# Optimization experiments

Hardware: AMD Instinct MI355X
Metric: run time of the kernel (lower is better)

## Reference

```python
import jax, jax.numpy as jnp
import numpy as np

N, E, F, H, G, U, A = 50000, 800000, 96, 96, 64, 32, 16


def _linear_params(key, fan_in, fan_out):
    # torch nn.Linear default init: U(-1/sqrt(fan_in), 1/sqrt(fan_in))
    s = 1.0 / np.sqrt(fan_in)
    kw, kb = jax.random.split(key)
    W = jax.random.uniform(kw, (fan_in, fan_out), jnp.float32, -s, s)
    b = jax.random.uniform(kb, (fan_out,), jnp.float32, -s, s)
    return W, b


def setup_inputs() -> dict:
    key = jax.random.key(0)
    ks = jax.random.split(key, 12)
    x = jax.random.normal(ks[0], (N, F), jnp.float32)
    edge_index = jax.random.randint(ks[1], (2, E), 0, N, dtype=jnp.int32)
    batch = jnp.sort(jax.random.randint(ks[2], (N,), 0, G, dtype=jnp.int32))
    u = jax.random.normal(ks[3], (G, U), jnp.float32)
    W1, b1 = _linear_params(ks[4], F, H)      # conv1
    W2, b2 = _linear_params(ks[5], H, H)      # conv2
    aW1, ab1 = _linear_params(ks[6], H + U, H)
    aW2, ab2 = _linear_params(ks[7], H, A)
    cW1, cb1 = _linear_params(ks[8], H + U, H)
    cW2, cb2 = _linear_params(ks[9], H, 1)
    return {"x": x, "edge_index": edge_index, "batch": batch, "u": u,
            "W1": W1, "b1": b1, "W2": W2, "b2": b2,
            "aW1": aW1, "ab1": ab1, "aW2": aW2, "ab2": ab2,
            "cW1": cW1, "cb1": cb1, "cW2": cW2, "cb2": cb2}


def reference(x, edge_index, batch, u, W1, b1, W2, b2,
              aW1, ab1, aW2, ab2, cW1, cb1, cW2, cb2):
    n = x.shape[0]
    src, dst = edge_index[0], edge_index[1]
    # GCN symmetric normalization with self-loops (PyG GCNConv defaults)
    deg = jnp.zeros((n,), x.dtype).at[dst].add(1.0) + 1.0  # +1 for self-loop
    dis = jax.lax.rsqrt(deg)                               # deg^{-1/2}
    edge_norm = (dis[src] * dis[dst])[:, None]             # [E,1]
    self_norm = (dis * dis)[:, None]                       # [N,1] = deg^{-1}

    def gcn(h, W, b):
        h = h @ W                                          # linear (bias after agg)
        agg = jax.ops.segment_sum(h[src] * edge_norm, dst, num_segments=n)
        return agg + h * self_norm + b

    h = jax.nn.relu(gcn(x, W1, b1))
    h = jax.nn.relu(gcn(h, W2, b2))

    # global mean pool over graphs
    cnt = jax.ops.segment_sum(jnp.ones((n,), h.dtype), batch, num_segments=G)
    pooled = jax.ops.segment_sum(h, batch, num_segments=G) / jnp.maximum(cnt, 1.0)[:, None]

    comb = jnp.concatenate([pooled, u], axis=1)            # [G, H+U]
    action_logits = jax.nn.relu(comb @ aW1 + ab1) @ aW2 + ab2   # [G, A]
    state_value = jax.nn.relu(comb @ cW1 + cb1) @ cW2 + cb2     # [G, 1]
    return action_logits, state_value
```

## Files before the change

### kernel.cpp

```cpp
#include <hip/hip_runtime.h>
#include <hip/hip_bf16.h>

#define FH 96
#define GU 32
#define GA 16
#define NG 64

typedef __attribute__((ext_vector_type(8))) short bf16x8;
typedef __attribute__((ext_vector_type(8))) unsigned short u16x8;
typedef __attribute__((ext_vector_type(4))) float f32x4;

static __device__ __forceinline__ unsigned short f2bf(float f) {
    unsigned int u = __float_as_uint(f);
    unsigned int r = (u + 0x7fffu + ((u >> 16) & 1u)) >> 16;
    return (unsigned short)r;
}
static __device__ __forceinline__ float bf2f(unsigned short h) {
    return __uint_as_float(((unsigned int)h) << 16);
}

__global__ void zero_k(float4* __restrict__ p, int n4) {
    int i = blockIdx.x * blockDim.x + threadIdx.x;
    if (i < n4) p[i] = make_float4(0.f, 0.f, 0.f, 0.f);
}

__global__ void count_deg_k(const int* __restrict__ dst, int* __restrict__ deg,
                            unsigned short* __restrict__ rank16, int E) {
    int e = blockIdx.x * blockDim.x + threadIdx.x;
    if (e < E) rank16[e] = (unsigned short)atomicAdd(&deg[dst[e]], 1);
}

__global__ __launch_bounds__(256) void partial_k(const int* __restrict__ deg,
                                                 int* __restrict__ blockSums, int n) {
    int base = blockIdx.x * 1024;
    int t = threadIdx.x;
    int s = 0;
#pragma unroll
    for (int j = 0; j < 4; j++) {
        int i = base + t * 4 + j;
        if (i < n) s += deg[i];
    }
    __shared__ int red[4];
    for (int off = 32; off > 0; off >>= 1) s += __shfl_down(s, off, 64);
    if ((t & 63) == 0) red[t >> 6] = s;
    __syncthreads();
    if (t == 0) blockSums[blockIdx.x] = red[0] + red[1] + red[2] + red[3];
}

__global__ __launch_bounds__(256) void emit_k(const int* __restrict__ deg,
                                              const int* __restrict__ blockSums,
                                              int* __restrict__ rowstart,
                                              float* __restrict__ dis,
                                              int n, int nb) {
    __shared__ int sh[256];
    int t = threadIdx.x;
    sh[t] = (t < nb) ? blockSums[t] : 0;
    __syncthreads();
    for (int off = 1; off < 256; off <<= 1) {
        int v = 0;
        if (t >= off) v = sh[t - off];
        __syncthreads();
        if (t >= off) sh[t] += v;
        __syncthreads();
    }
    int blockBase = (blockIdx.x == 0) ? 0 : sh[blockIdx.x - 1];
    __syncthreads();

    int base = blockIdx.x * 1024;
    int d[4];
    int s = 0;
#pragma unroll
    for (int j = 0; j < 4; j++) {
        int i = base + t * 4 + j;
        d[j] = (i < n) ? deg[i] : 0;
        s += d[j];
    }
    sh[t] = s;
    __syncthreads();
    for (int off = 1; off < 256; off <<= 1) {
        int v = 0;
        if (t >= off) v = sh[t - off];
        __syncthreads();
        if (t >= off) sh[t] += v;
        __syncthreads();
    }
    int run = blockBase + ((t == 0) ? 0 : sh[t - 1]);
#pragma unroll
    for (int j = 0; j < 4; j++) {
        int i = base + t * 4 + j;
        if (i < n) {
            rowstart[i] = run;
            dis[i] = rsqrtf((float)d[j] + 1.0f);
        }
        run += d[j];
    }
    if (blockIdx.x == gridDim.x - 1 && t == 255) rowstart[n] = run;
}

__global__ void fill_k(const int* __restrict__ src, const int* __restrict__ dst,
                       const int* __restrict__ rowstart,
                       const unsigned short* __restrict__ rank16,
                       unsigned short* __restrict__ csr, int E) {
    int e = blockIdx.x * blockDim.x + threadIdx.x;
    if (e < E) {
        int pos = rowstart[dst[e]] + (int)rank16[e];
        csr[pos] = (unsigned short)src[e];
    }
}

__global__ __launch_bounds__(256) void convW_k(const float* __restrict__ W1,
                                               const float* __restrict__ W2,
                                               unsigned short* __restrict__ WB1,
                                               unsigned short* __restrict__ WB2) {
    const float* W = (blockIdx.x == 0) ? W1 : W2;
    unsigned short* WB = (blockIdx.x == 0) ? WB1 : WB2;
    for (int idx = threadIdx.x; idx < 2 * 3 * 6 * 64 * 8; idx += 256) {
        int j = idx & 7;
        int lane = (idx >> 3) & 63;
        int frag = idx >> 9;
        int cg = frag % 6;
        int rest = frag / 6;
        int ks = rest % 3;
        int t = rest / 3;
        int k = ks * 32 + (lane >> 4) * 8 + j;
        int n = cg * 16 + (lane & 15);
        float w = W[k * FH + n];
        unsigned short h = f2bf(w);
        WB[idx] = (t == 0) ? h : f2bf(w - bf2f(h));
    }
}

template <int INMODE>
__global__ __launch_bounds__(256, 3) void gemm_mfma_k(
    const float* __restrict__ Xf, const unsigned short* __restrict__ Xb,
    const unsigned short* __restrict__ WB, const float* __restrict__ scale,
    unsigned short* __restrict__ Yb, int nrows) {
    int lane = threadIdx.x & 63;
    int wid  = threadIdx.x >> 6;
    int wr = wid >> 1, wc = wid & 1;
    int row0 = blockIdx.x * 64 + wr * 32;

    bf16x8 b[2][3][3];
#pragma unroll
    for (int t = 0; t < 2; t++)
#pragma unroll
        for (int ks = 0; ks < 3; ks++)
#pragma unroll
            for (int cg = 0; cg < 3; cg++) {
                int frag = (t * 3 + ks) * 6 + wc * 3 + cg;
                b[t][ks][cg] = *(const bf16x8*)(WB + frag * 512 + lane * 8);
            }

    f32x4 acc[2][3];
#pragma unroll
    for (int rg = 0; rg < 2; rg++)
#pragma unroll
        for (int cg = 0; cg < 3; cg++) acc[rg][cg] = (f32x4){0.f, 0.f, 0.f, 0.f};

    int r0 = lane & 15;
    int kcol = (lane >> 4) * 8;
#pragma unroll
    for (int ks = 0; ks < 3; ks++) {
        bf16x8 ah[2], al[2];
#pragma unroll
        for (int rg = 0; rg < 2; rg++) {
            if (INMODE == 1) {
                size_t off = (size_t)(row0 + rg * 16 + r0) * FH + ks * 32 + kcol;
                ah[rg] = *(const bf16x8*)(Xb + off);
            } else {
                int rr = row0 + rg * 16 + r0;
                if (rr >= nrows) rr = nrows - 1;
                const float* xp = Xf + (size_t)rr * FH + ks * 32 + kcol;
                float4 v0 = *(const float4*)xp;
                float4 v1 = *(const float4*)(xp + 4);
                float xv[8] = {v0.x, v0.y, v0.z, v0.w, v1.x, v1.y, v1.z, v1.w};
                bf16x8 hh, ll;
#pragma unroll
                for (int j = 0; j < 8; j++) {
                    unsigned short h = f2bf(xv[j]);
                    hh[j] = (short)h;
                    ll[j] = (short)f2bf(xv[j] - bf2f(h));
                }
                ah[rg] = hh;
                al[rg] = ll;
            }
        }
#pragma unroll
        for (int rg = 0; rg < 2; rg++)
#pragma unroll
            for (int cg = 0; cg < 3; cg++)
                acc[rg][cg] = __builtin_amdgcn_mfma_f32_16x16x32_bf16(
                    ah[rg], b[0][ks][cg], acc[rg][cg], 0, 0, 0);
#pragma unroll
        for (int rg = 0; rg < 2; rg++)
#pragma unroll
            for (int cg = 0; cg < 3; cg++)
                acc[rg][cg] = __builtin_amdgcn_mfma_f32_16x16x32_bf16(
                    ah[rg], b[1][ks][cg], acc[rg][cg], 0, 0, 0);
        if (INMODE == 0) {
#pragma unroll
            for (int rg = 0; rg < 2; rg++)
#pragma unroll
                for (int cg = 0; cg < 3; cg++)
                    acc[rg][cg] = __builtin_amdgcn_mfma_f32_16x16x32_bf16(
                        al[rg], b[0][ks][cg], acc[rg][cg], 0, 0, 0);
        }
    }

#pragma unroll
    for (int rg = 0; rg < 2; rg++) {
#pragma unroll
        for (int r = 0; r < 4; r++) {
            int row = row0 + rg * 16 + (lane >> 4) * 4 + r;
            if (row < nrows) {
                float s = scale[row];
#pragma unroll
                for (int cg = 0; cg < 3; cg++) {
                    int col = wc * 48 + cg * 16 + (lane & 15);
                    Yb[(size_t)row * FH + col] = f2bf(acc[rg][cg][r] * s);
                }
            }
        }
    }
}

__global__ __launch_bounds__(256) void gather12_k(
    const unsigned short* __restrict__ hXb, const float* __restrict__ dis,
    const int* __restrict__ rowstart, const unsigned short* __restrict__ csr,
    const float* __restrict__ bias, unsigned short* __restrict__ outB, int n) {
    int idx = blockIdx.x * blockDim.x + threadIdx.x;
    if (idx >= n * 12) return;
    int node = idx / 12;
    int f8 = (idx - node * 12) * 8;
    int s = rowstart[node];
    int e = rowstart[node + 1];
    u16x8 sv = *(const u16x8*)&hXb[node * FH + f8];
    float a[8];
#pragma unroll
    for (int j = 0; j < 8; j++) a[j] = bf2f((unsigned short)sv[j]);
    int p = s;
    for (; p + 8 <= e; p += 8) {
        int i0 = csr[p],     i1 = csr[p + 1], i2 = csr[p + 2], i3 = csr[p + 3];
        int i4 = csr[p + 4], i5 = csr[p + 5], i6 = csr[p + 6], i7 = csr[p + 7];
        u16x8 v0 = *(const u16x8*)&hXb[i0 * FH + f8];
        u16x8 v1 = *(const u16x8*)&hXb[i1 * FH + f8];
        u16x8 v2 = *(const u16x8*)&hXb[i2 * FH + f8];
        u16x8 v3 = *(const u16x8*)&hXb[i3 * FH + f8];
        u16x8 v4 = *(const u16x8*)&hXb[i4 * FH + f8];
        u16x8 v5 = *(const u16x8*)&hXb[i5 * FH + f8];
        u16x8 v6 = *(const u16x8*)&hXb[i6 * FH + f8];
        u16x8 v7 = *(const u16x8*)&hXb[i7 * FH + f8];
#pragma unroll
        for (int j = 0; j < 8; j++) {
            a[j] += ((bf2f((unsigned short)v0[j]) + bf2f((unsigned short)v1[j]))
                   + (bf2f((unsigned short)v2[j]) + bf2f((unsigned short)v3[j])))
                  + ((bf2f((unsigned short)v4[j]) + bf2f((unsigned short)v5[j]))
                   + (bf2f((unsigned short)v6[j]) + bf2f((unsigned short)v7[j])));
        }
    }
    for (; p + 4 <= e; p += 4) {
        int i0 = csr[p], i1 = csr[p + 1], i2 = csr[p + 2], i3 = csr[p + 3];
        u16x8 v0 = *(const u16x8*)&hXb[i0 * FH + f8];
        u16x8 v1 = *(const u16x8*)&hXb[i1 * FH + f8];
        u16x8 v2 = *(const u16x8*)&hXb[i2 * FH + f8];
        u16x8 v3 = *(const u16x8*)&hXb[i3 * FH + f8];
#pragma unroll
        for (int j = 0; j < 8; j++) {
            a[j] += (bf2f((unsigned short)v0[j]) + bf2f((unsigned short)v1[j]))
                  + (bf2f((unsigned short)v2[j]) + bf2f((unsigned short)v3[j]));
        }
    }
    for (; p < e; p++) {
        int i0 = csr[p];
        u16x8 v0 = *(const u16x8*)&hXb[i0 * FH + f8];
#pragma unroll
        for (int j = 0; j < 8; j++) a[j] += bf2f((unsigned short)v0[j]);
    }
    float dn = dis[node];
    float4 bv0 = *(const float4*)&bias[f8];
    float4 bv1 = *(const float4*)&bias[f8 + 4];
    float bb[8] = {bv0.x, bv0.y, bv0.z, bv0.w, bv1.x, bv1.y, bv1.z, bv1.w};
    u16x8 hh;
#pragma unroll
    for (int j = 0; j < 8; j++) hh[j] = f2bf(fmaxf(a[j] * dn + bb[j], 0.0f));
    *(u16x8*)&outB[node * FH + f8] = hh;
}

__global__ __launch_bounds__(128) void pool3_k(const unsigned short* __restrict__ h,
                                               const int* __restrict__ bat,
                                               float* __restrict__ pooled,
                                               float* __restrict__ cnt, int n) {
    const int CH = 32;
    int beg = blockIdx.x * CH;
    if (beg >= n) return;
    int end = min(beg + CH, n);
    int t = threadIdx.x;
    if (t < FH) {
        float acc = 0.f;
        int g = bat[beg];
        for (int node = beg; node < end; ++node) {
            int gg = bat[node];
            if (gg != g) { atomicAdd(&pooled[g * FH + t], acc); acc = 0.f; g = gg; }
            acc += bf2f(h[(size_t)node * FH + t]);
        }
        atomicAdd(&pooled[g * FH + t], acc);
    } else if (t == FH) {
        float c = 0.f;
        int g = bat[beg];
        for (int node = beg; node < end; ++node) {
            int gg = bat[node];
            if (gg != g) { atomicAdd(&cnt[g], c); c = 0.f; g = gg; }
            c += 1.f;
        }
        atomicAdd(&cnt[g], c);
    }
}

__global__ __launch_bounds__(128) void head_k(const float* __restrict__ pooled,
                                              const float* __restrict__ cnt,
                                              const float* __restrict__ u,
                                              const float* __restrict__ aW1, const float* __restrict__ ab1,
                                              const float* __restrict__ aW2, const float* __restrict__ ab2,
                                              const float* __restrict__ cW1, const float* __restrict__ cb1,
                                              const float* __restrict__ cW2, const float* __restrict__ cb2,
                                              float* __restrict__ out, int G) {
    int g = blockIdx.x;
    int t = threadIdx.x;
    __shared__ float comb[FH + GU];
    __shared__ float hidA[FH];
    __shared__ float hidC[FH];
    __shared__ float tmp[FH];
    float c = fmaxf(cnt[g], 1.0f);
    if (t < FH) comb[t] = pooled[g * FH + t] / c;
    else if (t < FH + GU) comb[t] = u[g * GU + (t - FH)];
    __syncthreads();
    if (t < FH) {
        float a = ab1[t], cc = cb1[t];
        for (int k = 0; k < FH + GU; k++) {
            float cv = comb[k];
            a += cv * aW1[k * FH + t];
            cc += cv * cW1[k * FH + t];
        }
        hidA[t] = fmaxf(a, 0.0f);
        hidC[t] = fmaxf(cc, 0.0f);
    }
    __syncthreads();
    if (t < GA) {
        float a = ab2[t];
        for (int j = 0; j < FH; j++) a += hidA[j] * aW2[j * GA + t];
        out[g * GA + t] = a;
    }
    if (t >= 32 && t < 32 + FH) tmp[t - 32] = hidC[t - 32] * cW2[t - 32];
    __syncthreads();
    if (t == 0) {
        float v = cb2[0];
        for (int j = 0; j < FH; j++) v += tmp[j];
        out[G * GA + g] = v;
    }
}

extern "C" void kernel_launch(void* const* d_in, const int* in_sizes, int n_in,
                              void* d_out, int out_size, void* d_ws, size_t ws_size,
                              hipStream_t stream) {
    const float* x   = (const float*)d_in[0];
    const int*   ei  = (const int*)d_in[1];
    const int*   bat = (const int*)d_in[2];
    const float* u   = (const float*)d_in[3];
    const float* W1  = (const float*)d_in[4];
    const float* b1  = (const float*)d_in[5];
    const float* W2  = (const float*)d_in[6];
    const float* b2  = (const float*)d_in[7];
    const float* aW1 = (const float*)d_in[8];
    const float* ab1 = (const float*)d_in[9];
    const float* aW2 = (const float*)d_in[10];
    const float* ab2 = (const float*)d_in[11];
    const float* cW1 = (const float*)d_in[12];
    const float* cb1 = (const float*)d_in[13];
    const float* cW2 = (const float*)d_in[14];
    const float* cb2 = (const float*)d_in[15];
    float* out = (float*)d_out;

    const int N = in_sizes[0] / FH;
    const int E = in_sizes[1] / 2;
    const int G = in_sizes[3] / GU;
    const int NPAD = (N + 63) / 64 * 64;

    const int* src = ei;
    const int* dst = ei + E;

    float* ws = (float*)d_ws;
    size_t o = 0;
    int*   degI     = (int*)(ws + o);   o += NPAD;
    float* pooled   = ws + o;           o += NG * FH;
    float* cnt      = ws + o;           o += 64;
    size_t zero_elems = o;
    float* dis      = ws + o;           o += NPAD;
    int*   rowstart = (int*)(ws + o);   o += NPAD;
    int*   blockSums= (int*)(ws + o);   o += 512;
    unsigned short* rank16 = (unsigned short*)(ws + o); o += ((size_t)(E + 1) / 2 + 63) / 64 * 64;
    unsigned short* csr16  = (unsigned short*)(ws + o); o += ((size_t)(E + 1) / 2 + 63) / 64 * 64;
    unsigned short* WB1 = (unsigned short*)(ws + o); o += 9216;
    unsigned short* WB2 = (unsigned short*)(ws + o); o += 9216;
    unsigned short* XhB = (unsigned short*)(ws + o); o += (size_t)NPAD * FH / 2;
    unsigned short* hXb = (unsigned short*)(ws + o); o += (size_t)NPAD * FH / 2;
    (void)ws_size;

    unsigned short* h2b = XhB;

    int gridE = (E + 255) / 256;
    int gridG12 = (N * 12 + 255) / 256;
    int gridMfma = NPAD / 64;
    int nbScan = (N + 1023) / 1024;
    int gridPool = (N + 31) / 32;
    int n4zero = (int)(zero_elems / 4);
    int gridZero = (n4zero + 255) / 256;

    zero_k<<<gridZero, 256, 0, stream>>>((float4*)ws, n4zero);

    count_deg_k<<<gridE, 256, 0, stream>>>(dst, degI, rank16, E);
    partial_k<<<nbScan, 256, 0, stream>>>(degI, blockSums, N);
    emit_k<<<nbScan, 256, 0, stream>>>(degI, blockSums, rowstart, dis, N, nbScan);
    fill_k<<<gridE, 256, 0, stream>>>(src, dst, rowstart, rank16, csr16, E);

    convW_k<<<2, 256, 0, stream>>>(W1, W2, WB1, WB2);

    gemm_mfma_k<0><<<gridMfma, 256, 0, stream>>>(x, (const unsigned short*)nullptr,
                                                 WB1, dis, hXb, N);
    gather12_k<<<gridG12, 256, 0, stream>>>(hXb, dis, rowstart, csr16, b1, XhB, N);
    gemm_mfma_k<1><<<gridMfma, 256, 0, stream>>>((const float*)nullptr, XhB,
                                                 WB2, dis, hXb, N);
    gather12_k<<<gridG12, 256, 0, stream>>>(hXb, dis, rowstart, csr16, b2, h2b, N);

    pool3_k<<<gridPool, 128, 0, stream>>>(h2b, bat, pooled, cnt, N);
    head_k<<<G, 128, 0, stream>>>(pooled, cnt, u, aW1, ab1, aW2, ab2,
                                  cW1, cb1, cW2, cb2, out, G);
}
```

Measured before the change: 180.1 us.

## Merge weight conversion into zeroing kernel and fold scan partials into emit

The weight bf16-split conversion moves into the zeroing kernel as two extra blocks, removing one launch. The separate partial-sum kernel is dropped: each emit block now recomputes its prefix by summing all degrees before its range and tree-reducing, trading one launch for redundant reads of up to about 50K ints per block. The CSR fill also switches to nontemporal stores.

```diff
diff --git a/kernel.cpp b/kernel.cpp
--- a/kernel.cpp
+++ b/kernel.cpp
@@ -19,9 +19,35 @@
     return __uint_as_float(((unsigned int)h) << 16);
 }
 
-__global__ void zero_k(float4* __restrict__ p, int n4) {
-    int i = blockIdx.x * blockDim.x + threadIdx.x;
-    if (i < n4) p[i] = make_float4(0.f, 0.f, 0.f, 0.f);
+__global__ __launch_bounds__(256) void init_k(float4* __restrict__ zp, int n4,
+                                              int nZeroBlocks,
+                                              const float* __restrict__ W1,
+                                              const float* __restrict__ W2,
+                                              unsigned short* __restrict__ WB1,
+                                              unsigned short* __restrict__ WB2) {
+    int b = blockIdx.x;
+    if (b < nZeroBlocks) {
+        int i = b * blockDim.x + threadIdx.x;
+        if (i < n4) zp[i] = make_float4(0.f, 0.f, 0.f, 0.f);
+    } else {
+        int half = b - nZeroBlocks;
+        const float* W = half ? W2 : W1;
+        unsigned short* WB = half ? WB2 : WB1;
+        for (int idx = threadIdx.x; idx < 2 * 3 * 6 * 64 * 8; idx += 256) {
+            int j = idx & 7;
+            int lane = (idx >> 3) & 63;
+            int frag = idx >> 9;
+            int cg = frag % 6;
+            int rest = frag / 6;
+            int ks = rest % 3;
+            int t = rest / 3;
+            int k = ks * 32 + (lane >> 4) * 8 + j;
+            int n = cg * 16 + (lane & 15);
+            float w = W[k * FH + n];
+            unsigned short h = f2bf(w);
+            WB[idx] = (t == 0) ? h : f2bf(w - bf2f(h));
+        }
+    }
 }
 
 __global__ void count_deg_k(const int* __restrict__ dst, int* __restrict__ deg,
@@ -30,43 +56,24 @@
     if (e < E) rank16[e] = (unsigned short)atomicAdd(&deg[dst[e]], 1);
 }
 
-__global__ __launch_bounds__(256) void partial_k(const int* __restrict__ deg,
-                                                 int* __restrict__ blockSums, int n) {
-    int base = blockIdx.x * 1024;
-    int t = threadIdx.x;
-    int s = 0;
-#pragma unroll
-    for (int j = 0; j < 4; j++) {
-        int i = base + t * 4 + j;
-        if (i < n) s += deg[i];
-    }
-    __shared__ int red[4];
-    for (int off = 32; off > 0; off >>= 1) s += __shfl_down(s, off, 64);
-    if ((t & 63) == 0) red[t >> 6] = s;
-    __syncthreads();
-    if (t == 0) blockSums[blockIdx.x] = red[0] + red[1] + red[2] + red[3];
-}
-
 __global__ __launch_bounds__(256) void emit_k(const int* __restrict__ deg,
-                                              const int* __restrict__ blockSums,
                                               int* __restrict__ rowstart,
-                                              float* __restrict__ dis,
-                                              int n, int nb) {
+                                              float* __restrict__ dis, int n) {
     __shared__ int sh[256];
     int t = threadIdx.x;
-    sh[t] = (t < nb) ? blockSums[t] : 0;
-    __syncthreads();
-    for (int off = 1; off < 256; off <<= 1) {
-        int v = 0;
-        if (t >= off) v = sh[t - off];
+    int base = blockIdx.x * 1024;
+
+    int pre = 0;
+    for (int i = t; i < base; i += 256) pre += deg[i];
+    sh[t] = pre;
+    __syncthreads();
+    for (int off = 128; off > 0; off >>= 1) {
+        if (t < off) sh[t] += sh[t + off];
         __syncthreads();
-        if (t >= off) sh[t] += v;
-        __syncthreads();
-    }
-    int blockBase = (blockIdx.x == 0) ? 0 : sh[blockIdx.x - 1];
-    __syncthreads();
-
-    int base = blockIdx.x * 1024;
+    }
+    int blockBase = sh[0];
+    __syncthreads();
+
     int d[4];
     int s = 0;
 #pragma unroll
@@ -104,29 +111,7 @@
     int e = blockIdx.x * blockDim.x + threadIdx.x;
     if (e < E) {
         int pos = rowstart[dst[e]] + (int)rank16[e];
-        csr[pos] = (unsigned short)src[e];
-    }
-}
-
-__global__ __launch_bounds__(256) void convW_k(const float* __restrict__ W1,
-                                               const float* __restrict__ W2,
-                                               unsigned short* __restrict__ WB1,
-                                               unsigned short* __restrict__ WB2) {
-    const float* W = (blockIdx.x == 0) ? W1 : W2;
-    unsigned short* WB = (blockIdx.x == 0) ? WB1 : WB2;
-    for (int idx = threadIdx.x; idx < 2 * 3 * 6 * 64 * 8; idx += 256) {
-        int j = idx & 7;
-        int lane = (idx >> 3) & 63;
-        int frag = idx >> 9;
-        int cg = frag % 6;
-        int rest = frag / 6;
-        int ks = rest % 3;
-        int t = rest / 3;
-        int k = ks * 32 + (lane >> 4) * 8 + j;
-        int n = cg * 16 + (lane & 15);
-        float w = W[k * FH + n];
-        unsigned short h = f2bf(w);
-        WB[idx] = (t == 0) ? h : f2bf(w - bf2f(h));
+        __builtin_nontemporal_store((unsigned short)src[e], &csr[pos]);
     }
 }
 
@@ -396,7 +381,6 @@
     size_t zero_elems = o;
     float* dis      = ws + o;           o += NPAD;
     int*   rowstart = (int*)(ws + o);   o += NPAD;
-    int*   blockSums= (int*)(ws + o);   o += 512;
     unsigned short* rank16 = (unsigned short*)(ws + o); o += ((size_t)(E + 1) / 2 + 63) / 64 * 64;
     unsigned short* csr16  = (unsigned short*)(ws + o); o += ((size_t)(E + 1) / 2 + 63) / 64 * 64;
     unsigned short* WB1 = (unsigned short*)(ws + o); o += 9216;
@@ -415,14 +399,12 @@
     int n4zero = (int)(zero_elems / 4);
     int gridZero = (n4zero + 255) / 256;
 
-    zero_k<<<gridZero, 256, 0, stream>>>((float4*)ws, n4zero);
+    init_k<<<gridZero + 2, 256, 0, stream>>>((float4*)ws, n4zero, gridZero,
+                                             W1, W2, WB1, WB2);
 
     count_deg_k<<<gridE, 256, 0, stream>>>(dst, degI, rank16, E);
-    partial_k<<<nbScan, 256, 0, stream>>>(degI, blockSums, N);
-    emit_k<<<nbScan, 256, 0, stream>>>(degI, blockSums, rowstart, dis, N, nbScan);
+    emit_k<<<nbScan, 256, 0, stream>>>(degI, rowstart, dis, N);
     fill_k<<<gridE, 256, 0, stream>>>(src, dst, rowstart, rank16, csr16, E);
-
-    convW_k<<<2, 256, 0, stream>>>(W1, W2, WB1, WB2);
 
     gemm_mfma_k<0><<<gridMfma, 256, 0, stream>>>(x, (const unsigned short*)nullptr,
                                                  WB1, dis, hXb, N);
```

Result: slower. 210.7 us (+17.0%).
